# Kernel optimization log

Measured on AMD Instinct MI355X. Metric: run time of the kernel, lower is better.

Reference implementation:

```python
import jax, jax.numpy as jnp
import numpy as np

B, T, H, C_CLS = 1024, 256, 256, 10
SIGMA = 1.0 / H


def setup_inputs() -> dict:
    key = jax.random.key(0)
    ks = jax.random.split(key, 10)
    n = lambda k, shp: SIGMA * jax.random.normal(k, shp, dtype=jnp.float32)
    return {
        "x": jax.random.normal(ks[0], (B, T), dtype=jnp.float32),
        "W_gx": n(ks[1], (1, H)), "W_gh": n(ks[2], (H, H)), "b_g": jnp.zeros(H, jnp.float32),
        "W_ix": n(ks[3], (1, H)), "W_ih": n(ks[4], (H, H)), "b_i": jnp.zeros(H, jnp.float32),
        "W_fx": n(ks[5], (1, H)), "W_fh": n(ks[6], (H, H)), "b_f": jnp.zeros(H, jnp.float32),
        "W_ox": n(ks[7], (1, H)), "W_oh": n(ks[8], (H, H)), "b_o": jnp.zeros(H, jnp.float32),
        "W_ph": n(ks[9], (H, C_CLS)), "b_p": jnp.zeros(C_CLS, jnp.float32),
    }


def reference(x, W_gx, W_gh, b_g, W_ix, W_ih, b_i, W_fx, W_fh, b_f, W_ox, W_oh, b_o, W_ph, b_p):
    batch = x.shape[0]
    hdim = W_gh.shape[0]

    def step(carry, x_t):
        h, c = carry
        xi = x_t[:, None]  # [B,1] scalar input per step
        g = jnp.tanh(xi @ W_gx + h @ W_gh + b_g)
        i = jax.nn.sigmoid(xi @ W_ix + h @ W_ih + b_i)
        # NOTE: original torch code swaps b_o/b_f in f_t/o_t; preserved faithfully.
        f = jax.nn.sigmoid(xi @ W_fx + h @ W_fh + b_o)
        o = jax.nn.sigmoid(xi @ W_ox + h @ W_oh + b_f)
        c = g * i + c * f
        h = jnp.tanh(c) * o
        return (h, c), None

    h0 = jnp.zeros((batch, hdim), x.dtype)
    c0 = jnp.zeros((batch, hdim), x.dtype)
    (h_T, _), _ = jax.lax.scan(step, (h0, c0), x.T)  # scan over time [T,B]
    # original computes p_t every step but only returns the last one
    return h_T @ W_ph + b_p
```

## Files before the change

kernel.cpp:

```cpp
#include <hip/hip_runtime.h>


#define Bsz   1024
#define Tt    256
#define Hh    256
#define NCLS  10
#define RGR   16
#define NRG   64
#define NCG   4
#define NTHR  1024
#define HSZ   ((size_t)Bsz * Hh)

typedef float f32x4 __attribute__((ext_vector_type(4)));
typedef short s16x8 __attribute__((ext_vector_type(8)));
typedef unsigned int u32;
typedef u32  u32x2 __attribute__((ext_vector_type(2)));
typedef unsigned long long u64;

#define PL1    0
#define PL2    8192
#define HOWNB  16384
#define HSTR   68
#define SMEMB  (16384 + 16 * HSTR * 4)

__device__ __forceinline__ unsigned short f2bf(float f) {
    u32 u = __builtin_bit_cast(u32, f);
    return (unsigned short)((u + 0x7FFFu + ((u >> 16) & 1u)) >> 16);
}
__device__ __forceinline__ float bf2f(unsigned short b) {
    u32 u = ((u32)b) << 16;
    return __builtin_bit_cast(float, u);
}
template<int CTRL>
__device__ __forceinline__ float quadf(float v) {
    return __builtin_bit_cast(float,
        __builtin_amdgcn_update_dpp(0, __builtin_bit_cast(int, v),
                                    CTRL, 0xF, 0xF, true));
}
__device__ __forceinline__ float fast_tanh(float v) {
    const float e = __expf(-2.0f * fabsf(v));
    const float t = (1.0f - e) * __builtin_amdgcn_rcpf(1.0f + e);
    return copysignf(t, v);
}
__device__ __forceinline__ u64 coh_load64(const u64* p) {
    return __hip_atomic_load((u64*)p, __ATOMIC_RELAXED, __HIP_MEMORY_SCOPE_AGENT);
}
__device__ __forceinline__ unsigned coh_load32(const unsigned* p) {
    return __hip_atomic_load((unsigned*)p, __ATOMIC_RELAXED, __HIP_MEMORY_SCOPE_AGENT);
}
__device__ __forceinline__ void coh_store32(u32* p, u32 v) {
    __hip_atomic_store(p, v, __ATOMIC_RELAXED, __HIP_MEMORY_SCOPE_AGENT);
}
__device__ __forceinline__ int swz(int ks, int krow) {
    return ((krow & 1) << 6) | ((ks & 1) << 5) | ((krow >> 1) << 4);
}

extern "C" __global__ void __launch_bounds__(NTHR, 4)
lstm_v12(const float* __restrict__ x,
         const float* __restrict__ W_gx, const float* __restrict__ W_gh, const float* __restrict__ b_g,
         const float* __restrict__ W_ix, const float* __restrict__ W_ih, const float* __restrict__ b_i,
         const float* __restrict__ W_fx, const float* __restrict__ W_fh, const float* __restrict__ b_f,
         const float* __restrict__ W_ox, const float* __restrict__ W_oh, const float* __restrict__ b_o,
         const float* __restrict__ W_ph, const float* __restrict__ b_p,
         float* __restrict__ out, u32* __restrict__ hpack, unsigned* __restrict__ fcnt)
{
    __shared__ __align__(16) char smem[SMEMB];
    u32* hown = (u32*)(smem + HOWNB);

    const int tid  = threadIdx.x;
    const int lane = tid & 63;
    const int wv   = tid >> 6;
    const int rg   = blockIdx.x & 63;
    const int cg   = blockIdx.x >> 6;
    const int r0   = rg * RGR;

    const int gate   = lane & 3;
    const int hcol_l = wv * 4 + ((lane & 15) >> 2);
    const int hcol_g = cg * 64 + hcol_l;
    const int krow   = lane >> 4;

    const float* __restrict__ Wg =
        (gate == 0) ? W_gh : (gate == 1) ? W_ih : (gate == 2) ? W_fh : W_oh;
    s16x8 bw1[8], bw2[8];
    #pragma unroll
    for (int ks = 0; ks < 8; ++ks) {
        s16x8 v1, v2;
        #pragma unroll
        for (int e = 0; e < 8; ++e) {
            const float w = Wg[(size_t)(ks * 32 + krow * 8 + e) * Hh + hcol_g];
            const unsigned short c1 = f2bf(w);
            const unsigned short c2 = f2bf(w - bf2f(c1));
            v1[e] = (short)c1; v2[e] = (short)c2;
        }
        bw1[ks] = v1; bw2[ks] = v2;
    }

    const float wx = ((gate == 0) ? W_gx : (gate == 1) ? W_ix : (gate == 2) ? W_fx : W_ox)[hcol_g];
    const float bb = ((gate == 0) ? b_g  : (gate == 1) ? b_i  : (gate == 2) ? b_o  : b_f )[hcol_g];
    float c_st[4];
    #pragma unroll
    for (int r = 0; r < 4; ++r) c_st[r] = 0.0f;

    const int s    = wv & 3;
    const int q    = wv >> 2;
    const int srow = q * 4 + krow;
    const int sc4  = (lane & 15) * 4;
    const int kg   = s * 64 + sc4;
    const int sks  = kg >> 5;
    const int skr  = (kg >> 3) & 3;
    const int se0  = kg & 7;
    const int swb  = (sks * 1024 + (skr * 16 + srow) * 16 + se0 * 2) ^ swz(sks, skr);

    unsigned* fbase = fcnt + rg * NCG;

    for (int i = tid; i < 16 * HSTR; i += NTHR) hown[i] = 0u;
    __syncthreads();

    for (int t = 0; t < Tt; ++t) {
        const u32* hcur = hpack + ((t & 1) ? HSZ : 0);
        u32*       hnxt = hpack + ((t & 1) ? 0 : HSZ);

        float xv[4];
        #pragma unroll
        for (int r = 0; r < 4; ++r)
            xv[r] = x[(size_t)(r0 + krow * 4 + r) * Tt + t];

        u32 v0, v1, v2, v3;
        if (s != cg) {
            if (t > 0)
                while (coh_load32(fbase + s) < (unsigned)t) __builtin_amdgcn_s_sleep(1);
            const u64* src = (const u64*)(hcur + (size_t)(r0 + srow) * Hh + s * 64 + sc4);
            const u64 q0 = coh_load64(src);
            const u64 q1 = coh_load64(src + 1);
            v0 = (u32)q0; v1 = (u32)(q0 >> 32);
            v2 = (u32)q1; v3 = (u32)(q1 >> 32);
        } else {
            const uint4 qq = *(const uint4*)(hown + srow * HSTR + sc4);
            v0 = qq.x; v1 = qq.y; v2 = qq.z; v3 = qq.w;
        }
        {
            u32x2 lo, hi;
            lo[0] = (v0 & 0xffffu) | (v1 << 16);
            lo[1] = (v2 & 0xffffu) | (v3 << 16);
            hi[0] = (v0 >> 16) | (v1 & 0xffff0000u);
            hi[1] = (v2 >> 16) | (v3 & 0xffff0000u);
            *(u32x2*)(smem + PL1 + swb) = lo;
            *(u32x2*)(smem + PL2 + swb) = hi;
        }
        __syncthreads();

        f32x4 aA = {0.f,0.f,0.f,0.f}, aB = {0.f,0.f,0.f,0.f}, aC = {0.f,0.f,0.f,0.f};
        #pragma unroll
        for (int ks = 0; ks < 8; ++ks) {
            const int off = (ks * 1024 + lane * 16) ^ swz(ks, krow);
            const s16x8 a1 = *(const s16x8*)(smem + PL1 + off);
            const s16x8 a2 = *(const s16x8*)(smem + PL2 + off);
            aA = __builtin_amdgcn_mfma_f32_16x16x32_bf16(a1, bw1[ks], aA, 0, 0, 0);
            aB = __builtin_amdgcn_mfma_f32_16x16x32_bf16(a2, bw1[ks], aB, 0, 0, 0);
            aC = __builtin_amdgcn_mfma_f32_16x16x32_bf16(a1, bw2[ks], aC, 0, 0, 0);
        }
        const f32x4 acc = aA + aB + aC;

        #pragma unroll
        for (int r = 0; r < 4; ++r) {
            const int row = krow * 4 + r;
            const float pre = acc[r] + fmaf(xv[r], wx, bb);
            const float vin = (gate == 0) ? 2.0f * pre : pre;
            const float e   = __expf(-fabsf(vin));
            const float rc  = __builtin_amdgcn_rcpf(1.0f + e);
            const float sig = (vin >= 0.0f) ? rc : 1.0f - rc;
            const float th  = copysignf((1.0f - e) * rc, pre);
            const float act = (gate == 0) ? th : sig;
            const float gv = quadf<0x00>(act);
            const float iv = quadf<0x55>(act);
            const float fv = quadf<0xAA>(act);
            const float ov = quadf<0xFF>(act);
            c_st[r] = fmaf(gv, iv, c_st[r] * fv);
            const float hv = fast_tanh(c_st[r]) * ov;
            if (gate == 0) {
                const unsigned short h1 = f2bf(hv);
                const unsigned short h2 = f2bf(hv - bf2f(h1));
                const u32 packed = (u32)h1 | ((u32)h2 << 16);
                coh_store32(&hnxt[(size_t)(r0 + row) * Hh + hcol_g], packed);
                hown[row * HSTR + hcol_l] = packed;
            }
        }

        asm volatile("s_waitcnt vmcnt(0)" ::: "memory");
        __syncthreads();
        if (tid == 0)
            __hip_atomic_store(fbase + cg, (unsigned)(t + 1),
                               __ATOMIC_RELEASE, __HIP_MEMORY_SCOPE_AGENT);
    }

    if (cg == 0) {
        for (int c = 1; c < NCG; ++c)
            while (coh_load32(fbase + c) < (unsigned)Tt) __builtin_amdgcn_s_sleep(1);
        u32* tile = (u32*)smem;
        const u64* src = (const u64*)(hpack + (size_t)r0 * Hh);
        for (int i = tid; i < 16 * 128; i += NTHR) {
            const u64 qv = coh_load64(src + i);
            tile[2 * i] = (u32)qv; tile[2 * i + 1] = (u32)(qv >> 32);
        }
        __syncthreads();
        for (int idx = tid; idx < RGR * NCLS; idx += NTHR) {
            const int row = idx / NCLS;
            const int cc  = idx - row * NCLS;
            float a = b_p[cc];
            for (int k = 0; k < Hh; ++k) {
                const u32 p = tile[row * Hh + k];
                a = fmaf(bf2f((unsigned short)p) + bf2f((unsigned short)(p >> 16)),
                         W_ph[k * NCLS + cc], a);
            }
            out[(size_t)(r0 + row) * NCLS + cc] = a;
        }
    }
}

extern "C" void kernel_launch(void* const* d_in, const int* in_sizes, int n_in,
                              void* d_out, int out_size, void* d_ws, size_t ws_size,
                              hipStream_t stream) {
    const float* x    = (const float*)d_in[0];
    const float* W_gx = (const float*)d_in[1];
    const float* W_gh = (const float*)d_in[2];
    const float* b_g  = (const float*)d_in[3];
    const float* W_ix = (const float*)d_in[4];
    const float* W_ih = (const float*)d_in[5];
    const float* b_i  = (const float*)d_in[6];
    const float* W_fx = (const float*)d_in[7];
    const float* W_fh = (const float*)d_in[8];
    const float* b_f  = (const float*)d_in[9];
    const float* W_ox = (const float*)d_in[10];
    const float* W_oh = (const float*)d_in[11];
    const float* b_o  = (const float*)d_in[12];
    const float* W_ph = (const float*)d_in[13];
    const float* b_p  = (const float*)d_in[14];
    float* out = (float*)d_out;

    u32*      hpack = (u32*)d_ws;
    unsigned* fcnt  = (unsigned*)((char*)d_ws + 2 * HSZ * sizeof(u32));
    const size_t clear_bytes = 2 * HSZ * sizeof(u32) + NRG * NCG * sizeof(unsigned);

    hipMemsetAsync(d_ws, 0, clear_bytes, stream);

    lstm_v12<<<dim3(NRG * NCG), dim3(NTHR), 0, stream>>>(
        x, W_gx, W_gh, b_g, W_ix, W_ih, b_i, W_fx, W_fh, b_f,
        W_ox, W_oh, b_o, W_ph, b_p, out, hpack, fcnt);
}
```

Before: 1.933 ms.

## Replace per-step flag barrier with timestamped h values and two-chunk interleaving

Replaces the per-column-group counter flags and release store with 64-bit hidden-state words that carry the timestep in their upper half, so consumers poll the data directly instead of a separate flag. Each block now owns 32 rows in two 16-row chunks and 32 columns with 512 threads, so one chunk's compute can overlap another block's production. The intent is to remove the vmcnt(0) drain and flag round-trip latency on the recurrent critical path. The cost is doubled h traffic, spin-polling on every h load, and 8 column groups to exchange with instead of 4.

```diff
diff --git a/kernel.cpp b/kernel.cpp
--- a/kernel.cpp
+++ b/kernel.cpp
@@ -5,23 +5,16 @@
 #define Tt    256
 #define Hh    256
 #define NCLS  10
-#define RGR   16
-#define NRG   64
-#define NCG   4
-#define NTHR  1024
-#define HSZ   ((size_t)Bsz * Hh)
+#define NTHR  512
+#define HSZ64 ((size_t)Bsz * Hh)
 
 typedef float f32x4 __attribute__((ext_vector_type(4)));
 typedef short s16x8 __attribute__((ext_vector_type(8)));
 typedef unsigned int u32;
-typedef u32  u32x2 __attribute__((ext_vector_type(2)));
 typedef unsigned long long u64;
 
-#define PL1    0
-#define PL2    8192
-#define HOWNB  16384
-#define HSTR   68
-#define SMEMB  (16384 + 16 * HSTR * 4)
+#define HOWNB  32768
+#define SMEMB  (32768 + 2 * 576 * 4)
 
 __device__ __forceinline__ unsigned short f2bf(float f) {
     u32 u = __builtin_bit_cast(u32, f);
@@ -45,24 +38,18 @@
 __device__ __forceinline__ u64 coh_load64(const u64* p) {
     return __hip_atomic_load((u64*)p, __ATOMIC_RELAXED, __HIP_MEMORY_SCOPE_AGENT);
 }
-__device__ __forceinline__ unsigned coh_load32(const unsigned* p) {
-    return __hip_atomic_load((unsigned*)p, __ATOMIC_RELAXED, __HIP_MEMORY_SCOPE_AGENT);
-}
-__device__ __forceinline__ void coh_store32(u32* p, u32 v) {
+__device__ __forceinline__ void coh_store64(u64* p, u64 v) {
     __hip_atomic_store(p, v, __ATOMIC_RELAXED, __HIP_MEMORY_SCOPE_AGENT);
 }
-__device__ __forceinline__ int swz(int ks, int krow) {
-    return ((krow & 1) << 6) | ((ks & 1) << 5) | ((krow >> 1) << 4);
-}
-
-extern "C" __global__ void __launch_bounds__(NTHR, 4)
-lstm_v12(const float* __restrict__ x,
+
+extern "C" __global__ void __launch_bounds__(NTHR, 2)
+lstm_v14(const float* __restrict__ x,
          const float* __restrict__ W_gx, const float* __restrict__ W_gh, const float* __restrict__ b_g,
          const float* __restrict__ W_ix, const float* __restrict__ W_ih, const float* __restrict__ b_i,
          const float* __restrict__ W_fx, const float* __restrict__ W_fh, const float* __restrict__ b_f,
          const float* __restrict__ W_ox, const float* __restrict__ W_oh, const float* __restrict__ b_o,
          const float* __restrict__ W_ph, const float* __restrict__ b_p,
-         float* __restrict__ out, u32* __restrict__ hpack, unsigned* __restrict__ fcnt)
+         float* __restrict__ out, u64* __restrict__ hx)
 {
     __shared__ __align__(16) char smem[SMEMB];
     u32* hown = (u32*)(smem + HOWNB);
@@ -70,13 +57,13 @@
     const int tid  = threadIdx.x;
     const int lane = tid & 63;
     const int wv   = tid >> 6;
-    const int rg   = blockIdx.x & 63;
-    const int cg   = blockIdx.x >> 6;
-    const int r0   = rg * RGR;
+    const int br   = blockIdx.x & 31;
+    const int cg   = blockIdx.x >> 5;
+    const int r0   = br * 32;
 
     const int gate   = lane & 3;
     const int hcol_l = wv * 4 + ((lane & 15) >> 2);
-    const int hcol_g = cg * 64 + hcol_l;
+    const int hcol_g = cg * 32 + hcol_l;
     const int krow   = lane >> 4;
 
     const float* __restrict__ Wg =
@@ -97,64 +84,60 @@
 
     const float wx = ((gate == 0) ? W_gx : (gate == 1) ? W_ix : (gate == 2) ? W_fx : W_ox)[hcol_g];
     const float bb = ((gate == 0) ? b_g  : (gate == 1) ? b_i  : (gate == 2) ? b_o  : b_f )[hcol_g];
-    float c_st[4];
+    float cA[4], cB[4];
     #pragma unroll
-    for (int r = 0; r < 4; ++r) c_st[r] = 0.0f;
-
-    const int s    = wv & 3;
-    const int q    = wv >> 2;
-    const int srow = q * 4 + krow;
-    const int sc4  = (lane & 15) * 4;
-    const int kg   = s * 64 + sc4;
-    const int sks  = kg >> 5;
-    const int skr  = (kg >> 3) & 3;
-    const int se0  = kg & 7;
-    const int swb  = (sks * 1024 + (skr * 16 + srow) * 16 + se0 * 2) ^ swz(sks, skr);
-
-    unsigned* fbase = fcnt + rg * NCG;
-
-    for (int i = tid; i < 16 * HSTR; i += NTHR) hown[i] = 0u;
+    for (int r = 0; r < 4; ++r) { cA[r] = 0.0f; cB[r] = 0.0f; }
+
+    const int sr = lane >> 2;
+    const int c8 = (lane & 3) * 8;
+
+    for (int i = tid; i < 2 * 576; i += NTHR) hown[i] = 0u;
     __syncthreads();
 
-    for (int t = 0; t < Tt; ++t) {
-        const u32* hcur = hpack + ((t & 1) ? HSZ : 0);
-        u32*       hnxt = hpack + ((t & 1) ? 0 : HSZ);
-
-        float xv[4];
-        #pragma unroll
-        for (int r = 0; r < 4; ++r)
-            xv[r] = x[(size_t)(r0 + krow * 4 + r) * Tt + t];
-
-        u32 v0, v1, v2, v3;
-        if (s != cg) {
-            if (t > 0)
-                while (coh_load32(fbase + s) < (unsigned)t) __builtin_amdgcn_s_sleep(1);
-            const u64* src = (const u64*)(hcur + (size_t)(r0 + srow) * Hh + s * 64 + sc4);
-            const u64 q0 = coh_load64(src);
-            const u64 q1 = coh_load64(src + 1);
-            v0 = (u32)q0; v1 = (u32)(q0 >> 32);
-            v2 = (u32)q1; v3 = (u32)(q1 >> 32);
+    auto substep = [&](int t, int ch, float* cst) {
+        u32 packed[8];
+        if (wv != cg) {
+            const u64* src = hx + (size_t)(t & 1) * HSZ64
+                           + (size_t)(r0 + ch * 16 + sr) * Hh + wv * 32 + c8;
+            u64 q[8];
+            for (;;) {
+                #pragma unroll
+                for (int i = 0; i < 8; ++i) q[i] = coh_load64(src + i);
+                bool ok = true;
+                #pragma unroll
+                for (int i = 0; i < 8; ++i) ok = ok && ((u32)(q[i] >> 32) == (u32)t);
+                if (__all(ok)) break;
+                __builtin_amdgcn_s_sleep(1);
+            }
+            #pragma unroll
+            for (int i = 0; i < 8; ++i) packed[i] = (u32)q[i];
         } else {
-            const uint4 qq = *(const uint4*)(hown + srow * HSTR + sc4);
-            v0 = qq.x; v1 = qq.y; v2 = qq.z; v3 = qq.w;
+            const u32* hp = hown + ch * 576 + sr * 36 + c8;
+            const uint4 q0 = *(const uint4*)hp;
+            const uint4 q1 = *(const uint4*)(hp + 4);
+            packed[0] = q0.x; packed[1] = q0.y; packed[2] = q0.z; packed[3] = q0.w;
+            packed[4] = q1.x; packed[5] = q1.y; packed[6] = q1.z; packed[7] = q1.w;
         }
         {
-            u32x2 lo, hi;
-            lo[0] = (v0 & 0xffffu) | (v1 << 16);
-            lo[1] = (v2 & 0xffffu) | (v3 << 16);
-            hi[0] = (v0 >> 16) | (v1 & 0xffff0000u);
-            hi[1] = (v2 >> 16) | (v3 & 0xffff0000u);
-            *(u32x2*)(smem + PL1 + swb) = lo;
-            *(u32x2*)(smem + PL2 + swb) = hi;
+            u32 lo[4], hi[4];
+            #pragma unroll
+            for (int i = 0; i < 4; ++i) {
+                const u32 p0 = packed[2 * i], p1 = packed[2 * i + 1];
+                lo[i] = (p0 & 0xffffu) | (p1 << 16);
+                hi[i] = (p0 >> 16)     | (p1 & 0xffff0000u);
+            }
+            char* pb = smem + ch * 16384 + wv * 1024 + ((((lane & 3) << 4) + sr) << 4);
+            *(uint4*)pb          = *(uint4*)lo;
+            *(uint4*)(pb + 8192) = *(uint4*)hi;
         }
         __syncthreads();
 
         f32x4 aA = {0.f,0.f,0.f,0.f}, aB = {0.f,0.f,0.f,0.f}, aC = {0.f,0.f,0.f,0.f};
         #pragma unroll
         for (int ks = 0; ks < 8; ++ks) {
-            const int off = (ks * 1024 + lane * 16) ^ swz(ks, krow);
-            const s16x8 a1 = *(const s16x8*)(smem + PL1 + off);
-            const s16x8 a2 = *(const s16x8*)(smem + PL2 + off);
+            const char* ab = smem + ch * 16384 + ks * 1024 + lane * 16;
+            const s16x8 a1 = *(const s16x8*)ab;
+            const s16x8 a2 = *(const s16x8*)(ab + 8192);
             aA = __builtin_amdgcn_mfma_f32_16x16x32_bf16(a1, bw1[ks], aA, 0, 0, 0);
             aB = __builtin_amdgcn_mfma_f32_16x16x32_bf16(a2, bw1[ks], aB, 0, 0, 0);
             aC = __builtin_amdgcn_mfma_f32_16x16x32_bf16(a1, bw2[ks], aC, 0, 0, 0);
@@ -163,47 +146,53 @@
 
         #pragma unroll
         for (int r = 0; r < 4; ++r) {
-            const int row = krow * 4 + r;
-            const float pre = acc[r] + fmaf(xv[r], wx, bb);
-            const float vin = (gate == 0) ? 2.0f * pre : pre;
-            const float e   = __expf(-fabsf(vin));
-            const float rc  = __builtin_amdgcn_rcpf(1.0f + e);
-            const float sig = (vin >= 0.0f) ? rc : 1.0f - rc;
-            const float th  = copysignf((1.0f - e) * rc, pre);
-            const float act = (gate == 0) ? th : sig;
+            const int rowl = krow * 4 + r;
+            const int row  = ch * 16 + rowl;
+            const float xval = x[(size_t)(r0 + row) * Tt + t];
+            const float pre  = acc[r] + fmaf(xval, wx, bb);
+            const float vin  = (gate == 0) ? 2.0f * pre : pre;
+            const float e    = __expf(-fabsf(vin));
+            const float rc   = __builtin_amdgcn_rcpf(1.0f + e);
+            const float sig  = (vin >= 0.0f) ? rc : 1.0f - rc;
+            const float th   = copysignf((1.0f - e) * rc, pre);
+            const float act  = (gate == 0) ? th : sig;
             const float gv = quadf<0x00>(act);
             const float iv = quadf<0x55>(act);
             const float fv = quadf<0xAA>(act);
             const float ov = quadf<0xFF>(act);
-            c_st[r] = fmaf(gv, iv, c_st[r] * fv);
-            const float hv = fast_tanh(c_st[r]) * ov;
+            cst[r] = fmaf(gv, iv, cst[r] * fv);
+            const float hv = fast_tanh(cst[r]) * ov;
             if (gate == 0) {
                 const unsigned short h1 = f2bf(hv);
                 const unsigned short h2 = f2bf(hv - bf2f(h1));
-                const u32 packed = (u32)h1 | ((u32)h2 << 16);
-                coh_store32(&hnxt[(size_t)(r0 + row) * Hh + hcol_g], packed);
-                hown[row * HSTR + hcol_l] = packed;
-            }
-        }
-
-        asm volatile("s_waitcnt vmcnt(0)" ::: "memory");
+                const u32 pk = (u32)h1 | ((u32)h2 << 16);
+                coh_store64(hx + (size_t)((t + 1) & 1) * HSZ64
+                               + (size_t)(r0 + row) * Hh + hcol_g,
+                            ((u64)(u32)(t + 1) << 32) | (u64)pk);
+                hown[ch * 576 + rowl * 36 + hcol_l] = pk;
+            }
+        }
+    };
+
+    for (int t = 0; t < Tt; ++t) {
+        substep(t, 0, cA);
+        substep(t, 1, cB);
+    }
+
+    if (cg == 0) {
         __syncthreads();
-        if (tid == 0)
-            __hip_atomic_store(fbase + cg, (unsigned)(t + 1),
-                               __ATOMIC_RELEASE, __HIP_MEMORY_SCOPE_AGENT);
-    }
-
-    if (cg == 0) {
-        for (int c = 1; c < NCG; ++c)
-            while (coh_load32(fbase + c) < (unsigned)Tt) __builtin_amdgcn_s_sleep(1);
         u32* tile = (u32*)smem;
-        const u64* src = (const u64*)(hpack + (size_t)r0 * Hh);
-        for (int i = tid; i < 16 * 128; i += NTHR) {
-            const u64 qv = coh_load64(src + i);
-            tile[2 * i] = (u32)qv; tile[2 * i + 1] = (u32)(qv >> 32);
+        const u64* src = hx + (size_t)r0 * Hh;
+        for (int i = tid; i < 32 * Hh; i += NTHR) {
+            u64 q = coh_load64(src + i);
+            while ((u32)(q >> 32) != (u32)Tt) {
+                __builtin_amdgcn_s_sleep(1);
+                q = coh_load64(src + i);
+            }
+            tile[i] = (u32)q;
         }
         __syncthreads();
-        for (int idx = tid; idx < RGR * NCLS; idx += NTHR) {
+        for (int idx = tid; idx < 32 * NCLS; idx += NTHR) {
             const int row = idx / NCLS;
             const int cc  = idx - row * NCLS;
             float a = b_p[cc];
@@ -237,13 +226,12 @@
     const float* b_p  = (const float*)d_in[14];
     float* out = (float*)d_out;
 
-    u32*      hpack = (u32*)d_ws;
-    unsigned* fcnt  = (unsigned*)((char*)d_ws + 2 * HSZ * sizeof(u32));
-    const size_t clear_bytes = 2 * HSZ * sizeof(u32) + NRG * NCG * sizeof(unsigned);
+    u64* hx = (u64*)d_ws;
+    const size_t clear_bytes = 2 * HSZ64 * sizeof(u64);
 
     hipMemsetAsync(d_ws, 0, clear_bytes, stream);
 
-    lstm_v12<<<dim3(NRG * NCG), dim3(NTHR), 0, stream>>>(
+    lstm_v14<<<dim3(256), dim3(NTHR), 0, stream>>>(
         x, W_gx, W_gh, b_g, W_ix, W_ih, b_i, W_fx, W_fh, b_f,
-        W_ox, W_oh, b_o, W_ph, b_p, out, hpack, fcnt);
-}
+        W_ox, W_oh, b_o, W_ph, b_p, out, hx);
+}
```

Measured after the change: 1.989 ms. +2.9%, slower.
